# Kernel tuning notes

Measured on AMD Instinct MI355X. Metric: run time of the kernel, lower is better.

## Reference

```python
import jax, jax.numpy as jnp
import numpy as np

N_HEADS = 8
N_POINTS = 4
LN_EPS = 1e-5


def _ln(x, g, b):
    m = jnp.mean(x, -1, keepdims=True)
    v = jnp.mean((x - m) ** 2, -1, keepdims=True)
    return (x - m) * jax.lax.rsqrt(v + LN_EPS) * g + b


def _mha(q, k, v, wq, bq, wk, bk, wv, bv, wo, bo):
    B, Lq, C = q.shape
    Dh = C // N_HEADS
    Q = (q @ wq.T + bq).reshape(B, Lq, N_HEADS, Dh)
    K = (k @ wk.T + bk).reshape(B, -1, N_HEADS, Dh)
    V = (v @ wv.T + bv).reshape(B, -1, N_HEADS, Dh)
    s = jnp.einsum('bqhd,bkhd->bhqk', Q, K) * (1.0 / float(np.sqrt(Dh)))
    a = jax.nn.softmax(s, -1)
    o = jnp.einsum('bhqk,bkhd->bqhd', a, V).reshape(B, Lq, C)
    return o @ wo.T + bo


def _ref_points(h, w, L):
    ry = jnp.linspace(0.5, h - 0.5, h) / h
    rx = jnp.linspace(0.5, w - 0.5, w) / w
    gy, gx = jnp.meshgrid(ry, rx, indexing='ij')
    ref = jnp.stack([gx.reshape(-1), gy.reshape(-1)], -1)[None]  # (1, h*w, 2)
    return jnp.broadcast_to(ref[:, :, None, :], (1, h * w, L, 2))


def _deform_core(value, shapes, starts, loc, aw):
    # value: (B, Len_in, H, Dh); loc: (B, Lq, H, L, P, 2); aw: (B, Lq, H, L, P)
    B, _, H, Dh = value.shape
    Lq, P = loc.shape[1], loc.shape[4]
    out = jnp.zeros((B, H, Lq, Dh), value.dtype)
    for l in range(shapes.shape[0]):
        Hl, Wl = int(shapes[l, 0]), int(shapes[l, 1])
        s = int(starts[l])
        v = value[:, s:s + Hl * Wl].transpose(0, 2, 1, 3)  # (B, H, Hl*Wl, Dh)
        # grid_sample(align_corners=False, padding_mode='zeros') pixel coords
        xl = loc[:, :, :, l, :, 0] * Wl - 0.5  # (B, Lq, H, P)
        yl = loc[:, :, :, l, :, 1] * Hl - 0.5
        x0 = jnp.floor(xl); y0 = jnp.floor(yl)
        fx = xl - x0; fy = yl - y0
        x0 = x0.astype(jnp.int32); y0 = y0.astype(jnp.int32)
        acc = jnp.zeros((B, H, Lq, P, Dh), value.dtype)
        for dy, dx in ((0, 0), (0, 1), (1, 0), (1, 1)):
            xi = x0 + dx; yi = y0 + dy
            wgt = (fx if dx else 1.0 - fx) * (fy if dy else 1.0 - fy)
            valid = ((xi >= 0) & (xi < Wl) & (yi >= 0) & (yi < Hl)).astype(value.dtype)
            idx = (jnp.clip(yi, 0, Hl - 1) * Wl + jnp.clip(xi, 0, Wl - 1))
            idx = idx.transpose(0, 2, 1, 3).reshape(B, H, Lq * P)
            g = jnp.take_along_axis(v, idx[..., None], axis=2).reshape(B, H, Lq, P, Dh)
            acc = acc + g * (wgt * valid).transpose(0, 2, 1, 3)[..., None]
        out = out + jnp.einsum('bhqpd,bqhp->bhqd', acc, aw[:, :, :, l])
    return out.transpose(0, 2, 1, 3).reshape(B, Lq, H * Dh)


def reference(tgt, query_pos, src, wq, bq, wk, bk, wv, bv, wo, bo, ln2_g, ln2_b,
              w_off, b_off, w_attn, b_attn, w_val, b_val, w_cout, b_cout,
              ln1_g, ln1_b, w1, b1, w2, b2, ln3_g, ln3_b,
              src_spatial_shapes, level_start_index, h, w):
    shapes = np.asarray(src_spatial_shapes)
    starts = np.asarray(level_start_index)
    h = int(h); w = int(w)
    L = shapes.shape[0]
    B, Lq, C = tgt.shape
    Dh = C // N_HEADS
    # --- self attention (post-LN residual) ---
    q = tgt + query_pos
    t2 = _mha(q, q, tgt, wq, bq, wk, bk, wv, bv, wo, bo)
    t = _ln(tgt + t2, ln2_g, ln2_b)
    # --- MSDeformAttn cross attention ---
    qc = t + query_pos
    value = (src @ w_val.T + b_val).reshape(B, -1, N_HEADS, Dh)
    off = (qc @ w_off.T + b_off).reshape(B, Lq, N_HEADS, L, N_POINTS, 2)
    aw = (qc @ w_attn.T + b_attn).reshape(B, Lq, N_HEADS, L * N_POINTS)
    aw = jax.nn.softmax(aw, -1).reshape(B, Lq, N_HEADS, L, N_POINTS)
    norm = jnp.stack([shapes[:, 1].astype(np.float32), shapes[:, 0].astype(np.float32)], -1)  # (L,2): (W,H)
    rp = _ref_points(h, w, L)  # (1, Lq, L, 2)
    loc = rp[:, :, None, :, None, :] + off / norm[None, None, None, :, None, :]
    samp = _deform_core(value, shapes, starts, loc, aw)
    t2 = samp @ w_cout.T + b_cout
    t = _ln(t + t2, ln1_g, ln1_b)
    # --- FFN ---
    t2 = jax.nn.relu(t @ w1.T + b1) @ w2.T + b2
    t = _ln(t + t2, ln3_g, ln3_b)
    return t


def setup_inputs() -> dict:
    key = jax.random.key(0)
    B, C, L, P, dff = 2, 256, 4, 4, 1024
    h = w = 48
    shapes = np.array([[48, 48], [24, 24], [12, 12], [6, 6]], np.int32)
    starts = np.array([0, 2304, 2880, 3024], np.int32)
    Len_in = 3060
    Lq = h * w
    ks = iter(jax.random.split(key, 40))
    def rn(shape, s=0.02):
        return jax.random.normal(next(ks), shape, jnp.float32) * s
    return dict(
        tgt=rn((B, Lq, C), 1.0), query_pos=rn((B, Lq, C), 1.0), src=rn((B, Len_in, C), 1.0),
        wq=rn((C, C)), bq=rn((C,)), wk=rn((C, C)), bk=rn((C,)), wv=rn((C, C)), bv=rn((C,)),
        wo=rn((C, C)), bo=rn((C,)),
        ln2_g=jnp.ones((C,)), ln2_b=jnp.zeros((C,)),
        w_off=rn((N_HEADS * L * P * 2, C)), b_off=rn((N_HEADS * L * P * 2,)),
        w_attn=rn((N_HEADS * L * P, C)), b_attn=rn((N_HEADS * L * P,)),
        w_val=rn((C, C)), b_val=rn((C,)), w_cout=rn((C, C)), b_cout=rn((C,)),
        ln1_g=jnp.ones((C,)), ln1_b=jnp.zeros((C,)),
        w1=rn((dff, C)), b1=rn((dff,)), w2=rn((C, dff)), b2=rn((C,)),
        ln3_g=jnp.ones((C,)), ln3_b=jnp.zeros((C,)),
        src_spatial_shapes=shapes, level_start_index=starts, h=h, w=w)
```

## Files before the change

kernel.cpp:

```cpp
#include <hip/hip_runtime.h>
#include <hip/hip_bf16.h>
#include <math.h>

typedef __hip_bfloat16 bf16;
typedef __attribute__((ext_vector_type(8))) short short8;
typedef __attribute__((ext_vector_type(4))) short short4v;
typedef __attribute__((ext_vector_type(4))) float f32x4;

static constexpr int B   = 2;
static constexpr int LQ  = 2304;
static constexpr int C   = 256;
static constexpr int NH  = 8;
static constexpr int DH  = 32;
static constexpr int NL  = 4;
static constexpr int NP  = 4;
static constexpr int LEN = 3060;
static constexpr int DFF = 1024;
static constexpr int MQ  = B * LQ;
static constexpr int MV  = B * LEN;
static constexpr int SZ1 = MQ * C;

#define MFMA16(a, b, c) __builtin_amdgcn_mfma_f32_16x16x32_bf16(a, b, c, 0, 0, 0)

__device__ __forceinline__ float ldf(const void* p, size_t i, int bf) {
  return bf ? __bfloat162float(((const bf16*)p)[i]) : ((const float*)p)[i];
}
__device__ __forceinline__ short fl2s(float v) {
  bf16 h = __float2bfloat16(v);
  return *(short*)&h;
}
__device__ __forceinline__ short fl2s_fast(float v) {
  union { float f; unsigned u; } x; x.f = v;
  return (short)((x.u + 0x8000u) >> 16);
}
__device__ __forceinline__ float s2fl(short s) {
  return __bfloat162float(*(bf16*)&s);
}
__device__ __forceinline__ int wire_is_bf16(const unsigned* gprobe) {
  return gprobe[0] == 0x3F803F80u;
}
__device__ __forceinline__ float ldbias(const void* b, int n, int fl) {
  return fl ? s2fl(((const short*)b)[n]) : s2fl(fl2s(((const float*)b)[n]));
}
__device__ __forceinline__ short8 add2bf(short8 a, short8 b) {
  short8 r;
#pragma unroll
  for (int j = 0; j < 8; ++j) r[j] = fl2s(s2fl(a[j]) + s2fl(b[j]));
  return r;
}

struct GemmJob {
  int Xmode;
  const short* Xbf; const void* Xwire; const void* Xwire2;
  const void* Wwire; const void* bwire;
  void* Y;
  int M, N, K, ldY, col0, relu, out_mode, nblk_x;
  float qscale;
};
struct GemmBatch { GemmJob j[4]; int start[5]; int njobs; };

template <int MR, int NR>
__global__ __launch_bounds__(256) void gemm_mfma(GemmBatch nb,
                                                 const unsigned* __restrict__ gprobe) {
  constexpr int MT = MR / 64;
  constexpr int NT_ = NR / 16;
  const int fl = wire_is_bf16(gprobe);
  int id = blockIdx.x;
  int jj = 0;
  while (jj + 1 < nb.njobs && id >= nb.start[jj + 1]) ++jj;
  const GemmJob jb = nb.j[jj];
  const int local = id - nb.start[jj];
  const int bx = local % jb.nblk_x;
  const int by = local / jb.nblk_x;
  const int M = jb.M, N = jb.N, K = jb.K;

  __shared__ short Xs[MR][72];
  __shared__ short Ws[NR][72];
  const int tid = threadIdx.x;
  const int wave = tid >> 6, lane = tid & 63;
  const int quad = lane >> 4, l16 = lane & 15;
  const int m0 = bx * MR, n0 = by * NR;
  f32x4 acc[MT][NT_];
#pragma unroll
  for (int mt = 0; mt < MT; ++mt)
#pragma unroll
    for (int nt = 0; nt < NT_; ++nt) acc[mt][nt] = f32x4{0.f, 0.f, 0.f, 0.f};

  const int xrow = (MR == 128) ? (tid >> 1) : (tid >> 2);
  const int xcol = (MR == 128) ? ((tid & 1) * 32) : ((tid & 3) * 16);
  constexpr int XU = (MR == 128) ? 4 : 2;
  const int wrow = (NR == 128) ? (tid >> 1) : (NR == 64) ? (tid >> 2) : (tid >> 3);
  const int wcol = (NR == 128) ? ((tid & 1) * 32)
                  : (NR == 64) ? ((tid & 3) * 16) : ((tid & 7) * 8);
  constexpr int WU = NR / 32;
  int xr = m0 + xrow; if (xr >= M) xr = M - 1;

  const short* xp16 = nullptr; const float* xpf = nullptr;
  const short* tp16 = nullptr; const short* pp16 = nullptr;
  const float* tpf  = nullptr; const float* ppf  = nullptr;
  if (jb.Xmode == 0) {
    xp16 = jb.Xbf + (size_t)xr * K;
  } else if (jb.Xmode == 2) {
    if (fl) xp16 = (const short*)jb.Xwire + (size_t)xr * K;
    else    xpf  = (const float*)jb.Xwire + (size_t)xr * K;
  } else {
    if (fl) { tp16 = (const short*)jb.Xwire + (size_t)xr * K;
              pp16 = (const short*)jb.Xwire2 + (size_t)xr * K; }
    else    { tpf  = (const float*)jb.Xwire + (size_t)xr * K;
              ppf  = (const float*)jb.Xwire2 + (size_t)xr * K; }
  }
  const short* wp16 = (const short*)jb.Wwire;
  const float* wpf  = (const float*)jb.Wwire;
  const size_t wro = (size_t)(n0 + wrow) * K;

  for (int k0 = 0; k0 < K; k0 += 64) {
    if (xp16) {
#pragma unroll
      for (int u = 0; u < XU; ++u)
        *(short8*)&Xs[xrow][xcol + u * 8] = *(const short8*)(xp16 + k0 + xcol + u * 8);
    } else if (xpf) {
#pragma unroll
      for (int u = 0; u < XU; ++u) {
        const float* s = xpf + k0 + xcol + u * 8;
        short8 r;
#pragma unroll
        for (int j = 0; j < 8; ++j) r[j] = fl2s(s[j]);
        *(short8*)&Xs[xrow][xcol + u * 8] = r;
      }
    } else if (tp16) {
#pragma unroll
      for (int u = 0; u < XU; ++u) {
        short8 t8 = *(const short8*)(tp16 + k0 + xcol + u * 8);
        short8 p8 = *(const short8*)(pp16 + k0 + xcol + u * 8);
        *(short8*)&Xs[xrow][xcol + u * 8] = add2bf(t8, p8);
      }
    } else {
#pragma unroll
      for (int u = 0; u < XU; ++u) {
        const float* t = tpf + k0 + xcol + u * 8;
        const float* p = ppf + k0 + xcol + u * 8;
        short8 r;
#pragma unroll
        for (int j = 0; j < 8; ++j) r[j] = fl2s(t[j] + p[j]);
        *(short8*)&Xs[xrow][xcol + u * 8] = r;
      }
    }
    if (fl) {
#pragma unroll
      for (int u = 0; u < WU; ++u)
        *(short8*)&Ws[wrow][wcol + u * 8] = *(const short8*)(wp16 + wro + k0 + wcol + u * 8);
    } else {
#pragma unroll
      for (int u = 0; u < WU; ++u) {
        const float* wp = wpf + wro + k0 + wcol + u * 8;
        short8 w;
#pragma unroll
        for (int j = 0; j < 8; ++j) w[j] = fl2s(wp[j]);
        *(short8*)&Ws[wrow][wcol + u * 8] = w;
      }
    }
    __syncthreads();
#pragma unroll
    for (int kc = 0; kc < 2; ++kc) {
      short8 bfr[NT_];
#pragma unroll
      for (int nt = 0; nt < NT_; ++nt)
        bfr[nt] = *(const short8*)&Ws[nt * 16 + l16][kc * 32 + quad * 8];
#pragma unroll
      for (int mt = 0; mt < MT; ++mt) {
        short8 a = *(const short8*)&Xs[wave * (16 * MT) + mt * 16 + l16][kc * 32 + quad * 8];
#pragma unroll
        for (int nt = 0; nt < NT_; ++nt)
          acc[mt][nt] = MFMA16(a, bfr[nt], acc[mt][nt]);
      }
    }
    __syncthreads();
  }

  if (jb.out_mode == 2) {
#pragma unroll
    for (int mt = 0; mt < MT; ++mt) {
      const int mbase = m0 + wave * (16 * MT) + mt * 16 + quad * 4;
      const int b = mbase / LQ;
      const int qb_ = mbase - b * LQ;
#pragma unroll
      for (int nt = 0; nt < NT_; ++nt) {
        const int n = n0 + nt * 16 + l16;
        const float bv = ldbias(jb.bwire, n, fl);
        short4v v4;
#pragma unroll
        for (int r = 0; r < 4; ++r) v4[r] = fl2s(acc[mt][nt][r] + bv);
        *(short4v*)((short*)jb.Y + (size_t)(b * 256 + n) * LQ + qb_) = v4;
      }
    }
    return;
  }
#pragma unroll
  for (int mt = 0; mt < MT; ++mt)
#pragma unroll
    for (int nt = 0; nt < NT_; ++nt) {
      const int n = n0 + nt * 16 + l16;
      const float bv = ldbias(jb.bwire, n, fl);
#pragma unroll
      for (int r = 0; r < 4; ++r) {
        const int m = m0 + wave * (16 * MT) + mt * 16 + quad * 4 + r;
        if (m < M) {
          float v = (acc[mt][nt][r] + bv) * jb.qscale;
          if (jb.relu) v = fmaxf(v, 0.f);
          if (jb.out_mode == 1)
            ((short*)jb.Y)[(size_t)m * jb.ldY + jb.col0 + n] = fl2s(v);
          else
            ((float*)jb.Y)[(size_t)m * jb.ldY + jb.col0 + n] = v;
        }
      }
    }
}

__global__ __launch_bounds__(256) void ln_kern(const void* __restrict__ A, int a_mode,
                                               const float* __restrict__ R,
                                               const void* __restrict__ g,
                                               const void* __restrict__ be,
                                               float* __restrict__ Yf32,
                                               short* __restrict__ Y16,
                                               void* __restrict__ Yfinal,
                                               const void* __restrict__ pos,
                                               short* __restrict__ Yqc,
                                               int rows, const unsigned* __restrict__ gprobe) {
  const int fl = wire_is_bf16(gprobe);
  const int row = blockIdx.x * 4 + (threadIdx.x >> 6);
  const int lane = threadIdx.x & 63;
  if (row >= rows) return;
  const int c0 = lane * 4;
  const size_t base = (size_t)row * C + c0;

  float x[4];
  if (a_mode == 1 && fl) {
    short4v a4 = *(const short4v*)((const short*)A + base);
#pragma unroll
    for (int j = 0; j < 4; ++j) x[j] = s2fl(a4[j]);
  } else {
    f32x4 a4 = *(const f32x4*)((const float*)A + base);
#pragma unroll
    for (int j = 0; j < 4; ++j) x[j] = a4[j];
  }
  f32x4 r4 = *(const f32x4*)(R + base);
  float s = 0.f, s2 = 0.f;
#pragma unroll
  for (int j = 0; j < 4; ++j) { x[j] += r4[j]; s += x[j]; s2 += x[j] * x[j]; }
#pragma unroll
  for (int off = 32; off > 0; off >>= 1) {
    s += __shfl_xor(s, off);
    s2 += __shfl_xor(s2, off);
  }
  const float mean = s * (1.f / C);
  const float var = fmaxf(s2 * (1.f / C) - mean * mean, 0.f);
  const float inv = rsqrtf(var + 1e-5f);

  float gv[4], bvv[4];
  if (fl) {
    short4v g4 = *(const short4v*)((const short*)g + c0);
    short4v b4 = *(const short4v*)((const short*)be + c0);
#pragma unroll
    for (int j = 0; j < 4; ++j) { gv[j] = s2fl(g4[j]); bvv[j] = s2fl(b4[j]); }
  } else {
    f32x4 g4 = *(const f32x4*)((const float*)g + c0);
    f32x4 b4 = *(const f32x4*)((const float*)be + c0);
#pragma unroll
    for (int j = 0; j < 4; ++j) { gv[j] = g4[j]; bvv[j] = b4[j]; }
  }
  float y[4];
#pragma unroll
  for (int j = 0; j < 4; ++j) y[j] = (x[j] - mean) * inv * gv[j] + bvv[j];

  if (Yfinal) {
    if (fl) {
      short4v o;
#pragma unroll
      for (int j = 0; j < 4; ++j) o[j] = fl2s(y[j]);
      *(short4v*)((short*)Yfinal + base) = o;
    } else {
      f32x4 o;
#pragma unroll
      for (int j = 0; j < 4; ++j) o[j] = y[j];
      *(f32x4*)((float*)Yfinal + base) = o;
    }
    return;
  }
  if (Yf32) {
    f32x4 o;
#pragma unroll
    for (int j = 0; j < 4; ++j) o[j] = y[j];
    *(f32x4*)(Yf32 + base) = o;
  }
  if (Y16) {
    short4v o;
#pragma unroll
    for (int j = 0; j < 4; ++j) o[j] = fl2s(y[j]);
    *(short4v*)(Y16 + base) = o;
  }
  if (Yqc) {
    float pv[4];
    if (fl) {
      short4v p4 = *(const short4v*)((const short*)pos + base);
#pragma unroll
      for (int j = 0; j < 4; ++j) pv[j] = s2fl(p4[j]);
    } else {
      f32x4 p4 = *(const f32x4*)((const float*)pos + base);
#pragma unroll
      for (int j = 0; j < 4; ++j) pv[j] = p4[j];
    }
    short4v o;
#pragma unroll
    for (int j = 0; j < 4; ++j) o[j] = fl2s(y[j] + pv[j]);
    *(short4v*)(Yqc + base) = o;
  }
}

__global__ __launch_bounds__(256) void flash_attn(const short* __restrict__ QK,
                                                  const short* __restrict__ Vt,
                                                  short* __restrict__ Op) {
  constexpr int LDQK = 512;
  constexpr int NC = LQ / 64;
  constexpr int NQT = 3;
  const int qb = blockIdx.x;
  const int bh = blockIdx.y;
  const int b = bh >> 3, h = bh & 7;
  const int tid = threadIdx.x;
  const int wave = tid >> 6, lane = tid & 63;
  const int quad = lane >> 4, l16 = lane & 15;

  __shared__ short Ps[4][16][68];
  __shared__ float lsh[256];

  const int q0 = qb * 48;
  const size_t rowb = (size_t)(b * LQ);
  const short* kcol = QK + 256 + h * DH + quad * 8;
  const short* vt0 = Vt + (size_t)(b * 256 + h * 32 + l16) * LQ + quad * 8;
  const short* vt1 = Vt + (size_t)(b * 256 + h * 32 + 16 + l16) * LQ + quad * 8;

  short8 qfrag[NQT];
#pragma unroll
  for (int qt = 0; qt < NQT; ++qt)
    qfrag[qt] = *(const short8*)(QK + (rowb + q0 + qt * 16 + l16) * LDQK + h * DH + quad * 8);

  f32x4 o0[NQT], o1[NQT];
  float lrow[NQT];
#pragma unroll
  for (int qt = 0; qt < NQT; ++qt) {
    o0[qt] = f32x4{0.f, 0.f, 0.f, 0.f};
    o1[qt] = f32x4{0.f, 0.f, 0.f, 0.f};
    lrow[qt] = 0.f;
  }

  short8 kf[4], vf[4];
  {
    const int k0 = wave * 64;
#pragma unroll
    for (int kt = 0; kt < 4; ++kt)
      kf[kt] = *(const short8*)(kcol + (rowb + k0 + kt * 16 + l16) * LDQK);
    vf[0] = *(const short8*)(vt0 + k0);
    vf[1] = *(const short8*)(vt0 + k0 + 32);
    vf[2] = *(const short8*)(vt1 + k0);
    vf[3] = *(const short8*)(vt1 + k0 + 32);
  }

  for (int c = wave; c < NC; c += 4) {
    short8 kn[4], vn[4];
    if (c + 4 < NC) {
      const int k0n = (c + 4) * 64;
#pragma unroll
      for (int kt = 0; kt < 4; ++kt)
        kn[kt] = *(const short8*)(kcol + (rowb + k0n + kt * 16 + l16) * LDQK);
      vn[0] = *(const short8*)(vt0 + k0n);
      vn[1] = *(const short8*)(vt0 + k0n + 32);
      vn[2] = *(const short8*)(vt1 + k0n);
      vn[3] = *(const short8*)(vt1 + k0n + 32);
    }

#pragma unroll
    for (int qt = 0; qt < NQT; ++qt) {
      f32x4 s[4];
#pragma unroll
      for (int kt = 0; kt < 4; ++kt) {
        f32x4 z = {0.f, 0.f, 0.f, 0.f};
        s[kt] = MFMA16(kf[kt], qfrag[qt], z);
      }

      float ps = 0.f;
#pragma unroll
      for (int kt = 0; kt < 4; ++kt)
#pragma unroll
        for (int r = 0; r < 4; ++r) {
          float p = __expf(s[kt][r]);
          s[kt][r] = p;
          ps += p;
        }
      lrow[qt] += ps;

#pragma unroll
      for (int kt = 0; kt < 4; ++kt) {
        short4v pk;
#pragma unroll
        for (int r = 0; r < 4; ++r) pk[r] = fl2s_fast(s[kt][r]);
        *(short4v*)&Ps[wave][l16][kt * 16 + quad * 4] = pk;
      }

#pragma unroll
      for (int half = 0; half < 2; ++half) {
        short4v a0 = *(const short4v*)&Ps[wave][l16][half * 32 + quad * 8];
        short4v a1 = *(const short4v*)&Ps[wave][l16][half * 32 + quad * 8 + 4];
        short8 afrag;
#pragma unroll
        for (int j = 0; j < 4; ++j) { afrag[j] = a0[j]; afrag[4 + j] = a1[j]; }
        o0[qt] = MFMA16(afrag, vf[half], o0[qt]);
        o1[qt] = MFMA16(afrag, vf[2 + half], o1[qt]);
      }
    }

#pragma unroll
    for (int kt = 0; kt < 4; ++kt) { kf[kt] = kn[kt]; vf[kt] = vn[kt]; }
  }

  float* obuf = (float*)&Ps[0][0][0];
  for (int qt = 0; qt < NQT; ++qt) {
    __syncthreads();
    lsh[(wave * 4 + quad) * 16 + l16] = lrow[qt];
#pragma unroll
    for (int r = 0; r < 4; ++r) {
      const int q = quad * 4 + r;
      obuf[(wave * 16 + q) * 32 + l16] = o0[qt][r];
      obuf[(wave * 16 + q) * 32 + 16 + l16] = o1[qt][r];
    }
    __syncthreads();
#pragma unroll
    for (int e = tid; e < 512; e += 256) {
      const int q = e >> 5, d = e & 31;
      float lg = 0.f;
#pragma unroll
      for (int i = 0; i < 16; ++i) lg += lsh[i * 16 + q];
      float ov = 0.f;
#pragma unroll
      for (int w = 0; w < 4; ++w) ov += obuf[(w * 16 + q) * 32 + d];
      Op[(rowb + q0 + qt * 16 + q) * C + h * DH + d] = fl2s_fast(ov / lg);
    }
  }
}

__global__ __launch_bounds__(256) void deform_kern(const short* __restrict__ value,
                                                   const float* __restrict__ oa,
                                                   const int* __restrict__ shapes,
                                                   const int* __restrict__ starts,
                                                   const int* __restrict__ hp,
                                                   const int* __restrict__ wp,
                                                   short* __restrict__ samp) {
  const int bq = blockIdx.x * 4 + (threadIdx.x >> 6);
  const int b = bq / LQ, q = bq % LQ;
  const int lane = threadIdx.x & 63;
  const int h_ = lane >> 3;
  const int d0 = (lane & 7) * 4;

  const int w0 = *wp, h0 = *hp;
  const int qx = q % w0, qy = q / w0;
  const float refx = (qx + 0.5f) / (float)w0;
  const float refy = (qy + 0.5f) / (float)h0;

  const float* offp = oa + (size_t)bq * 384 + h_ * 32;
  const float* awraw = oa + (size_t)bq * 384 + 256 + h_ * 16;

  float e[16];
  float mm = -1e30f;
#pragma unroll
  for (int j = 0; j < 16; ++j) mm = fmaxf(mm, awraw[j]);
  float ssum = 0.f;
#pragma unroll
  for (int j = 0; j < 16; ++j) {
    e[j] = __expf(awraw[j] - mm);
    ssum += e[j];
  }
  const float sinv = 1.f / ssum;

  float acc0 = 0.f, acc1 = 0.f, acc2 = 0.f, acc3 = 0.f;
  for (int l = 0; l < NL; ++l) {
    const int Hl = shapes[l * 2 + 0];
    const int Wl = shapes[l * 2 + 1];
    const int st = starts[l];
    const short* vbase = value + ((size_t)(b * LEN + st)) * C + h_ * DH + d0;
#pragma unroll
    for (int p = 0; p < NP; ++p) {
      const float ox = offp[l * 8 + p * 2 + 0];
      const float oy = offp[l * 8 + p * 2 + 1];
      const float a = e[l * 4 + p] * sinv;
      const float xl = refx * Wl + ox - 0.5f;
      const float yl = refy * Hl + oy - 0.5f;
      const float x0f = floorf(xl), y0f = floorf(yl);
      const float fx = xl - x0f, fy = yl - y0f;
      const int x0 = (int)x0f, y0 = (int)y0f;
#pragma unroll
      for (int corner = 0; corner < 4; ++corner) {
        const int dx = corner & 1, dy = corner >> 1;
        const int xi = x0 + dx, yi = y0 + dy;
        const float wx = dx ? fx : 1.f - fx;
        const float wy = dy ? fy : 1.f - fy;
        const bool valid = (xi >= 0) & (xi < Wl) & (yi >= 0) & (yi < Hl);
        if (valid) {
          const float w = a * wx * wy;
          short4v v4 = *(const short4v*)(vbase + (size_t)(yi * Wl + xi) * C);
          acc0 += w * s2fl(v4[0]);
          acc1 += w * s2fl(v4[1]);
          acc2 += w * s2fl(v4[2]);
          acc3 += w * s2fl(v4[3]);
        }
      }
    }
  }
  short4v out;
  out[0] = fl2s(acc0); out[1] = fl2s(acc1); out[2] = fl2s(acc2); out[3] = fl2s(acc3);
  *(short4v*)(samp + (size_t)bq * C + h_ * DH + d0) = out;
}

extern "C" void kernel_launch(void* const* d_in, const int* in_sizes, int n_in,
                              void* d_out, int out_size, void* d_ws, size_t ws_size,
                              hipStream_t stream) {
  const void* tgt       = d_in[0];
  const void* query_pos = d_in[1];
  const void* src       = d_in[2];
  const void* wq = d_in[3];  const void* bq = d_in[4];
  const void* wk = d_in[5];  const void* bk = d_in[6];
  const void* wv = d_in[7];  const void* bv = d_in[8];
  const void* wo = d_in[9];  const void* bo = d_in[10];
  const void* ln2_g = d_in[11]; const void* ln2_b = d_in[12];
  const void* w_off = d_in[13]; const void* b_off = d_in[14];
  const void* w_attn = d_in[15]; const void* b_attn = d_in[16];
  const void* w_val = d_in[17]; const void* b_val = d_in[18];
  const void* w_cout = d_in[19]; const void* b_cout = d_in[20];
  const void* ln1_g = d_in[21]; const void* ln1_b = d_in[22];
  const void* w1 = d_in[23]; const void* b1 = d_in[24];
  const void* w2 = d_in[25]; const void* b2 = d_in[26];
  const void* ln3_g = d_in[27]; const void* ln3_b = d_in[28];
  const int* shapes = (const int*)d_in[29];
  const int* starts = (const int*)d_in[30];
  const int* hp = (const int*)d_in[31];
  const int* wp = (const int*)d_in[32];
  const unsigned* gprobe = (const unsigned*)ln2_g;

  short* q16    = (short*)((char*)d_ws + 256);
  short* qk_out = q16 + SZ1;
  short* vt16   = qk_out + (size_t)MQ * 512;
  short* ao16   = vt16 + SZ1;
  short* valb   = ao16 + SZ1;
  short* ffn1   = valb + (size_t)MV * C;
  short* t1_16  = ffn1 + (size_t)MQ * DFF;
  float* t2a    = (float*)(t1_16 + SZ1);
  float* t_32   = t2a + SZ1;
  float* t1_32  = t_32 + SZ1;
  float* oa     = t1_32 + SZ1;

  const float scale = 1.f / sqrtf((float)DH);
  const dim3 blk(256);
  const int NX128 = MQ / 128;
  const int NX64  = MQ / 64;
  const int NXV   = (MV + 127) / 128;

  {
    GemmBatch nb;
    nb.njobs = 4;
    nb.j[0] = {4, nullptr, tgt, query_pos, wq, bq, qk_out,
               MQ, 256, 256, 512, 0, 0, 1, NX128, scale};
    nb.j[1] = {4, nullptr, tgt, query_pos, wk, bk, qk_out,
               MQ, 256, 256, 512, 256, 0, 1, NX128, 1.f};
    nb.j[2] = {2, nullptr, tgt, nullptr, wv, bv, vt16,
               MQ, 256, 256, 0, 0, 0, 2, NX128, 1.f};
    nb.j[3] = {2, nullptr, src, nullptr, w_val, b_val, valb,
               MV, 256, 256, 256, 0, 0, 1, NXV, 1.f};
    nb.start[0] = 0;
    nb.start[1] = NX128 * 4;
    nb.start[2] = nb.start[1] + NX128 * 4;
    nb.start[3] = nb.start[2] + NX128 * 4;
    nb.start[4] = nb.start[3] + NXV * 4;
    gemm_mfma<128, 64><<<nb.start[4], blk, 0, stream>>>(nb, gprobe);
  }
  flash_attn<<<dim3(LQ / 48, B * NH), blk, 0, stream>>>(qk_out, vt16, ao16);

  {
    GemmBatch nb;
    nb.njobs = 1;
    nb.j[0] = {0, ao16, nullptr, nullptr, wo, bo, t2a,
               MQ, 256, 256, 256, 0, 0, 0, NX64, 1.f};
    nb.start[0] = 0; nb.start[1] = NX64 * 8;
    gemm_mfma<64, 32><<<nb.start[1], blk, 0, stream>>>(nb, gprobe);
  }
  ln_kern<<<MQ / 4, blk, 0, stream>>>(tgt, 1, t2a, ln2_g, ln2_b,
                                      t_32, nullptr, nullptr, query_pos, q16, MQ, gprobe);

  {
    GemmBatch nb;
    nb.njobs = 2;
    nb.j[0] = {0, q16, nullptr, nullptr, w_off, b_off, oa,
               MQ, 256, 256, 384, 0, 0, 0, NX64, 1.f};
    nb.j[1] = {0, q16, nullptr, nullptr, w_attn, b_attn, oa,
               MQ, 128, 256, 384, 256, 0, 0, NX64, 1.f};
    nb.start[0] = 0;
    nb.start[1] = NX64 * 8;
    nb.start[2] = nb.start[1] + NX64 * 4;
    gemm_mfma<64, 32><<<nb.start[2], blk, 0, stream>>>(nb, gprobe);
  }
  deform_kern<<<MQ / 4, blk, 0, stream>>>(valb, oa, shapes, starts, hp, wp, ao16);

  {
    GemmBatch nb;
    nb.njobs = 1;
    nb.j[0] = {0, ao16, nullptr, nullptr, w_cout, b_cout, t2a,
               MQ, 256, 256, 256, 0, 0, 0, NX64, 1.f};
    nb.start[0] = 0; nb.start[1] = NX64 * 8;
    gemm_mfma<64, 32><<<nb.start[1], blk, 0, stream>>>(nb, gprobe);
  }
  ln_kern<<<MQ / 4, blk, 0, stream>>>(t_32, 2, t2a, ln1_g, ln1_b,
                                      t1_32, t1_16, nullptr, nullptr, nullptr, MQ, gprobe);

  {
    GemmBatch nb;
    nb.njobs = 1;
    nb.j[0] = {0, t1_16, nullptr, nullptr, w1, b1, ffn1,
               MQ, 1024, 256, 1024, 0, 1, 1, NX128, 1.f};
    nb.start[0] = 0; nb.start[1] = NX128 * 16;
    gemm_mfma<128, 64><<<nb.start[1], blk, 0, stream>>>(nb, gprobe);
  }
  {
    GemmBatch nb;
    nb.njobs = 1;
    nb.j[0] = {0, ffn1, nullptr, nullptr, w2, b2, t2a,
               MQ, 256, 1024, 256, 0, 0, 0, NX64, 1.f};
    nb.start[0] = 0; nb.start[1] = NX64 * 4;
    gemm_mfma<64, 64><<<nb.start[1], blk, 0, stream>>>(nb, gprobe);
  }
  ln_kern<<<MQ / 4, blk, 0, stream>>>(t1_32, 2, t2a, ln3_g, ln3_b,
                                      nullptr, nullptr, d_out, nullptr, nullptr, MQ, gprobe);
}
```

Baseline: 278.1 us.

## Fuse all layer stages into one cooperative persistent kernel with grid syncs

Replaces the eleven separate kernel launches (GEMMs, flash attention, layernorms, deformable sampling) with a single cooperative persistent kernel. Each stage loops over virtual blocks and stages are separated by grid-wide barriers, so launch overhead and inter-kernel gaps go away. The costs are a shared-memory footprint sized for the largest stage, occupancy limited by the biggest stage's register use, and the time spent in ten grid barriers. The FFN2 GEMM now runs with the 64x32 tile instead of 64x64.

```diff
diff --git a/kernel.cpp b/kernel.cpp
--- a/kernel.cpp
+++ b/kernel.cpp
@@ -1,6 +1,9 @@
 #include <hip/hip_runtime.h>
+#include <hip/hip_cooperative_groups.h>
 #include <hip/hip_bf16.h>
 #include <math.h>
+
+namespace cg = cooperative_groups;
 
 typedef __hip_bfloat16 bf16;
 typedef __attribute__((ext_vector_type(8))) short short8;
@@ -48,6 +51,11 @@
   for (int j = 0; j < 8; ++j) r[j] = fl2s(s2fl(a[j]) + s2fl(b[j]));
   return r;
 }
+__device__ __forceinline__ void gsync() {
+  __threadfence();
+  cg::this_grid().sync();
+  __threadfence();
+}
 
 struct GemmJob {
   int Xmode;
@@ -60,22 +68,18 @@
 struct GemmBatch { GemmJob j[4]; int start[5]; int njobs; };
 
 template <int MR, int NR>
-__global__ __launch_bounds__(256) void gemm_mfma(GemmBatch nb,
-                                                 const unsigned* __restrict__ gprobe) {
+__device__ void gemm_dev(const GemmBatch& nb, int id, int fl,
+                         short (*Xs)[72], short (*Ws)[72]) {
   constexpr int MT = MR / 64;
   constexpr int NT_ = NR / 16;
-  const int fl = wire_is_bf16(gprobe);
-  int id = blockIdx.x;
   int jj = 0;
   while (jj + 1 < nb.njobs && id >= nb.start[jj + 1]) ++jj;
   const GemmJob jb = nb.j[jj];
   const int local = id - nb.start[jj];
   const int bx = local % jb.nblk_x;
   const int by = local / jb.nblk_x;
-  const int M = jb.M, N = jb.N, K = jb.K;
-
-  __shared__ short Xs[MR][72];
-  __shared__ short Ws[NR][72];
+  const int M = jb.M, K = jb.K;
+
   const int tid = threadIdx.x;
   const int wave = tid >> 6, lane = tid & 63;
   const int quad = lane >> 4, l16 = lane & 15;
@@ -216,20 +220,15 @@
     }
 }
 
-__global__ __launch_bounds__(256) void ln_kern(const void* __restrict__ A, int a_mode,
-                                               const float* __restrict__ R,
-                                               const void* __restrict__ g,
-                                               const void* __restrict__ be,
-                                               float* __restrict__ Yf32,
-                                               short* __restrict__ Y16,
-                                               void* __restrict__ Yfinal,
-                                               const void* __restrict__ pos,
-                                               short* __restrict__ Yqc,
-                                               int rows, const unsigned* __restrict__ gprobe) {
-  const int fl = wire_is_bf16(gprobe);
-  const int row = blockIdx.x * 4 + (threadIdx.x >> 6);
+__device__ void ln_dev(const void* __restrict__ A, int a_mode,
+                       const float* __restrict__ R,
+                       const void* __restrict__ g, const void* __restrict__ be,
+                       float* __restrict__ Yf32, short* __restrict__ Y16,
+                       void* __restrict__ Yfinal,
+                       const void* __restrict__ pos, short* __restrict__ Yqc,
+                       int vb, int fl) {
+  const int row = vb * 4 + ((int)threadIdx.x >> 6);
   const int lane = threadIdx.x & 63;
-  if (row >= rows) return;
   const int c0 = lane * 4;
   const size_t base = (size_t)row * C + c0;
 
@@ -316,21 +315,19 @@
   }
 }
 
-__global__ __launch_bounds__(256) void flash_attn(const short* __restrict__ QK,
-                                                  const short* __restrict__ Vt,
-                                                  short* __restrict__ Op) {
+__device__ void flash_dev(const short* __restrict__ QK, const short* __restrict__ Vt,
+                          short* __restrict__ Op, int vb,
+                          short* __restrict__ ps, float* __restrict__ lsh) {
   constexpr int LDQK = 512;
   constexpr int NC = LQ / 64;
   constexpr int NQT = 3;
-  const int qb = blockIdx.x;
-  const int bh = blockIdx.y;
+  const int qb = vb % (LQ / 48);
+  const int bh = vb / (LQ / 48);
   const int b = bh >> 3, h = bh & 7;
   const int tid = threadIdx.x;
   const int wave = tid >> 6, lane = tid & 63;
   const int quad = lane >> 4, l16 = lane & 15;
-
-  __shared__ short Ps[4][16][68];
-  __shared__ float lsh[256];
+  short* Prow = ps + (wave * 16 + l16) * 68;
 
   const int q0 = qb * 48;
   const size_t rowb = (size_t)(b * LQ);
@@ -386,29 +383,29 @@
         s[kt] = MFMA16(kf[kt], qfrag[qt], z);
       }
 
-      float ps = 0.f;
+      float psum = 0.f;
 #pragma unroll
       for (int kt = 0; kt < 4; ++kt)
 #pragma unroll
         for (int r = 0; r < 4; ++r) {
           float p = __expf(s[kt][r]);
           s[kt][r] = p;
-          ps += p;
+          psum += p;
         }
-      lrow[qt] += ps;
+      lrow[qt] += psum;
 
 #pragma unroll
       for (int kt = 0; kt < 4; ++kt) {
         short4v pk;
 #pragma unroll
         for (int r = 0; r < 4; ++r) pk[r] = fl2s_fast(s[kt][r]);
-        *(short4v*)&Ps[wave][l16][kt * 16 + quad * 4] = pk;
+        *(short4v*)&Prow[kt * 16 + quad * 4] = pk;
       }
 
 #pragma unroll
       for (int half = 0; half < 2; ++half) {
-        short4v a0 = *(const short4v*)&Ps[wave][l16][half * 32 + quad * 8];
-        short4v a1 = *(const short4v*)&Ps[wave][l16][half * 32 + quad * 8 + 4];
+        short4v a0 = *(const short4v*)&Prow[half * 32 + quad * 8];
+        short4v a1 = *(const short4v*)&Prow[half * 32 + quad * 8 + 4];
         short8 afrag;
 #pragma unroll
         for (int j = 0; j < 4; ++j) { afrag[j] = a0[j]; afrag[4 + j] = a1[j]; }
@@ -421,7 +418,7 @@
     for (int kt = 0; kt < 4; ++kt) { kf[kt] = kn[kt]; vf[kt] = vn[kt]; }
   }
 
-  float* obuf = (float*)&Ps[0][0][0];
+  float* obuf = (float*)ps;
   for (int qt = 0; qt < NQT; ++qt) {
     __syncthreads();
     lsh[(wave * 4 + quad) * 16 + l16] = lrow[qt];
@@ -444,16 +441,14 @@
       Op[(rowb + q0 + qt * 16 + q) * C + h * DH + d] = fl2s_fast(ov / lg);
     }
   }
-}
-
-__global__ __launch_bounds__(256) void deform_kern(const short* __restrict__ value,
-                                                   const float* __restrict__ oa,
-                                                   const int* __restrict__ shapes,
-                                                   const int* __restrict__ starts,
-                                                   const int* __restrict__ hp,
-                                                   const int* __restrict__ wp,
-                                                   short* __restrict__ samp) {
-  const int bq = blockIdx.x * 4 + (threadIdx.x >> 6);
+  __syncthreads();
+}
+
+__device__ void deform_dev(const short* __restrict__ value, const float* __restrict__ oa,
+                           const int* __restrict__ shapes, const int* __restrict__ starts,
+                           const int* __restrict__ hp, const int* __restrict__ wp,
+                           short* __restrict__ samp, int vb) {
+  const int bq = vb * 4 + ((int)threadIdx.x >> 6);
   const int b = bq / LQ, q = bq % LQ;
   const int lane = threadIdx.x & 63;
   const int h_ = lane >> 3;
@@ -516,6 +511,61 @@
   short4v out;
   out[0] = fl2s(acc0); out[1] = fl2s(acc1); out[2] = fl2s(acc2); out[3] = fl2s(acc3);
   *(short4v*)(samp + (size_t)bq * C + h_ * DH + d0) = out;
+}
+
+struct MegaArgs {
+  GemmBatch gA, gWo, gOff, gCout, gF1, gF2;
+  const void* tgt; const void* qpos;
+  const void* ln2_g; const void* ln2_b;
+  const void* ln1_g; const void* ln1_b;
+  const void* ln3_g; const void* ln3_b;
+  float* t2a; float* t_32; float* t1_32;
+  short* q16; short* t1_16;
+  void* d_out;
+  const short* qk_out; const short* vt16; short* ao16;
+  const short* valb; const float* oa;
+  const int* shapes; const int* starts; const int* hp; const int* wp;
+  const unsigned* gprobe;
+  int nA, nWo, nOff, nCout, nF1, nF2;
+};
+
+__global__ __launch_bounds__(256) void mega(MegaArgs a) {
+  __shared__ alignas(16) short smemS[13824];
+  const int fl = wire_is_bf16(a.gprobe);
+  const int g0 = blockIdx.x, gs = gridDim.x;
+
+  for (int vb = g0; vb < a.nA; vb += gs)
+    gemm_dev<128, 64>(a.gA, vb, fl, (short(*)[72])smemS, (short(*)[72])(smemS + 128 * 72));
+  gsync();
+  for (int vb = g0; vb < (LQ / 48) * B * NH; vb += gs)
+    flash_dev(a.qk_out, a.vt16, a.ao16, vb, smemS, (float*)(smemS + 4352));
+  gsync();
+  for (int vb = g0; vb < a.nWo; vb += gs)
+    gemm_dev<64, 32>(a.gWo, vb, fl, (short(*)[72])smemS, (short(*)[72])(smemS + 64 * 72));
+  gsync();
+  for (int vb = g0; vb < MQ / 4; vb += gs)
+    ln_dev(a.tgt, 1, a.t2a, a.ln2_g, a.ln2_b, a.t_32, nullptr, nullptr, a.qpos, a.q16, vb, fl);
+  gsync();
+  for (int vb = g0; vb < a.nOff; vb += gs)
+    gemm_dev<64, 32>(a.gOff, vb, fl, (short(*)[72])smemS, (short(*)[72])(smemS + 64 * 72));
+  gsync();
+  for (int vb = g0; vb < MQ / 4; vb += gs)
+    deform_dev(a.valb, a.oa, a.shapes, a.starts, a.hp, a.wp, a.ao16, vb);
+  gsync();
+  for (int vb = g0; vb < a.nCout; vb += gs)
+    gemm_dev<64, 32>(a.gCout, vb, fl, (short(*)[72])smemS, (short(*)[72])(smemS + 64 * 72));
+  gsync();
+  for (int vb = g0; vb < MQ / 4; vb += gs)
+    ln_dev(a.t_32, 2, a.t2a, a.ln1_g, a.ln1_b, a.t1_32, a.t1_16, nullptr, nullptr, nullptr, vb, fl);
+  gsync();
+  for (int vb = g0; vb < a.nF1; vb += gs)
+    gemm_dev<128, 64>(a.gF1, vb, fl, (short(*)[72])smemS, (short(*)[72])(smemS + 128 * 72));
+  gsync();
+  for (int vb = g0; vb < a.nF2; vb += gs)
+    gemm_dev<64, 32>(a.gF2, vb, fl, (short(*)[72])smemS, (short(*)[72])(smemS + 64 * 72));
+  gsync();
+  for (int vb = g0; vb < MQ / 4; vb += gs)
+    ln_dev(a.t1_32, 2, a.t2a, a.ln3_g, a.ln3_b, nullptr, nullptr, a.d_out, nullptr, nullptr, vb, fl);
 }
 
 extern "C" void kernel_launch(void* const* d_in, const int* in_sizes, int n_in,
@@ -556,13 +606,13 @@
   float* oa     = t1_32 + SZ1;
 
   const float scale = 1.f / sqrtf((float)DH);
-  const dim3 blk(256);
   const int NX128 = MQ / 128;
   const int NX64  = MQ / 64;
   const int NXV   = (MV + 127) / 128;
 
+  MegaArgs ma;
   {
-    GemmBatch nb;
+    GemmBatch& nb = ma.gA;
     nb.njobs = 4;
     nb.j[0] = {4, nullptr, tgt, query_pos, wq, bq, qk_out,
                MQ, 256, 256, 512, 0, 0, 1, NX128, scale};
@@ -577,23 +627,18 @@
     nb.start[2] = nb.start[1] + NX128 * 4;
     nb.start[3] = nb.start[2] + NX128 * 4;
     nb.start[4] = nb.start[3] + NXV * 4;
-    gemm_mfma<128, 64><<<nb.start[4], blk, 0, stream>>>(nb, gprobe);
-  }
-  flash_attn<<<dim3(LQ / 48, B * NH), blk, 0, stream>>>(qk_out, vt16, ao16);
-
+    ma.nA = nb.start[4];
+  }
   {
-    GemmBatch nb;
+    GemmBatch& nb = ma.gWo;
     nb.njobs = 1;
     nb.j[0] = {0, ao16, nullptr, nullptr, wo, bo, t2a,
                MQ, 256, 256, 256, 0, 0, 0, NX64, 1.f};
     nb.start[0] = 0; nb.start[1] = NX64 * 8;
-    gemm_mfma<64, 32><<<nb.start[1], blk, 0, stream>>>(nb, gprobe);
-  }
-  ln_kern<<<MQ / 4, blk, 0, stream>>>(tgt, 1, t2a, ln2_g, ln2_b,
-                                      t_32, nullptr, nullptr, query_pos, q16, MQ, gprobe);
-
+    ma.nWo = nb.start[1];
+  }
   {
-    GemmBatch nb;
+    GemmBatch& nb = ma.gOff;
     nb.njobs = 2;
     nb.j[0] = {0, q16, nullptr, nullptr, w_off, b_off, oa,
                MQ, 256, 256, 384, 0, 0, 0, NX64, 1.f};
@@ -602,37 +647,49 @@
     nb.start[0] = 0;
     nb.start[1] = NX64 * 8;
     nb.start[2] = nb.start[1] + NX64 * 4;
-    gemm_mfma<64, 32><<<nb.start[2], blk, 0, stream>>>(nb, gprobe);
-  }
-  deform_kern<<<MQ / 4, blk, 0, stream>>>(valb, oa, shapes, starts, hp, wp, ao16);
-
+    ma.nOff = nb.start[2];
+  }
   {
-    GemmBatch nb;
+    GemmBatch& nb = ma.gCout;
     nb.njobs = 1;
     nb.j[0] = {0, ao16, nullptr, nullptr, w_cout, b_cout, t2a,
                MQ, 256, 256, 256, 0, 0, 0, NX64, 1.f};
     nb.start[0] = 0; nb.start[1] = NX64 * 8;
-    gemm_mfma<64, 32><<<nb.start[1], blk, 0, stream>>>(nb, gprobe);
-  }
-  ln_kern<<<MQ / 4, blk, 0, stream>>>(t_32, 2, t2a, ln1_g, ln1_b,
-                                      t1_32, t1_16, nullptr, nullptr, nullptr, MQ, gprobe);
-
+    ma.nCout = nb.start[1];
+  }
   {
-    GemmBatch nb;
+    GemmBatch& nb = ma.gF1;
     nb.njobs = 1;
     nb.j[0] = {0, t1_16, nullptr, nullptr, w1, b1, ffn1,
                MQ, 1024, 256, 1024, 0, 1, 1, NX128, 1.f};
     nb.start[0] = 0; nb.start[1] = NX128 * 16;
-    gemm_mfma<128, 64><<<nb.start[1], blk, 0, stream>>>(nb, gprobe);
+    ma.nF1 = nb.start[1];
   }
   {
-    GemmBatch nb;
+    GemmBatch& nb = ma.gF2;
     nb.njobs = 1;
     nb.j[0] = {0, ffn1, nullptr, nullptr, w2, b2, t2a,
                MQ, 256, 1024, 256, 0, 0, 0, NX64, 1.f};
-    nb.start[0] = 0; nb.start[1] = NX64 * 4;
-    gemm_mfma<64, 64><<<nb.start[1], blk, 0, stream>>>(nb, gprobe);
-  }
-  ln_kern<<<MQ / 4, blk, 0, stream>>>(t1_32, 2, t2a, ln3_g, ln3_b,
-                                      nullptr, nullptr, d_out, nullptr, nullptr, MQ, gprobe);
-}
+    nb.start[0] = 0; nb.start[1] = NX64 * 8;
+    ma.nF2 = nb.start[1];
+  }
+  ma.tgt = tgt; ma.qpos = query_pos;
+  ma.ln2_g = ln2_g; ma.ln2_b = ln2_b;
+  ma.ln1_g = ln1_g; ma.ln1_b = ln1_b;
+  ma.ln3_g = ln3_g; ma.ln3_b = ln3_b;
+  ma.t2a = t2a; ma.t_32 = t_32; ma.t1_32 = t1_32;
+  ma.q16 = q16; ma.t1_16 = t1_16;
+  ma.d_out = d_out;
+  ma.qk_out = qk_out; ma.vt16 = vt16; ma.ao16 = ao16;
+  ma.valb = valb; ma.oa = oa;
+  ma.shapes = shapes; ma.starts = starts; ma.hp = hp; ma.wp = wp;
+  ma.gprobe = gprobe;
+
+  int occ = 0;
+  hipOccupancyMaxActiveBlocksPerMultiprocessor(&occ, mega, 256, 0);
+  if (occ < 1) occ = 1;
+  int grid = occ * 256;
+  if (grid > MQ / 4) grid = MQ / 4;
+  void* params[] = {(void*)&ma};
+  hipLaunchCooperativeKernel(mega, dim3(grid), dim3(256), params, 0, stream);
+}
```

Measured after the change: 1.095 ms. 294% more time.
